# Kernel tuning notes

Measured on AMD Instinct MI355X. Metric: run time of the kernel, lower is better.

Reference implementation:

```python
import jax, jax.numpy as jnp
import numpy as np

NUM_HEADS = 16
DIM = 1024
N_TOKENS = 2048
S0 = 8            # number of frames
P = N_TOKENS // S0  # tokens per frame
B = 1


def setup_inputs() -> dict:
    key = jax.random.key(0)
    ks = jax.random.split(key, 8)
    C = DIM
    x = jax.random.normal(ks[0], (B, N_TOKENS, C), dtype=jnp.float32)
    # nn.Linear-style weights (out_features, in_features), scaled ~1/sqrt(fan_in)
    Wqkv = jax.random.normal(ks[1], (3 * C, C), dtype=jnp.float32) * (C ** -0.5)
    bqkv = jnp.zeros((3 * C,), dtype=jnp.float32)
    Wproj = jax.random.normal(ks[2], (C, C), dtype=jnp.float32) * (C ** -0.5)
    bproj = jnp.zeros((C,), dtype=jnp.float32)
    frame_bias = jax.random.normal(ks[3], (S0, S0), dtype=jnp.float32) * 0.5
    # frame adjacency: random sparsity pattern, diagonal always allowed
    adj = jax.random.bernoulli(ks[4], 0.25, (S0, S0))
    adj = adj | jnp.eye(S0, dtype=bool)
    frame_ids = (jnp.arange(N_TOKENS) // P).astype(jnp.int64)
    is_hub = jax.random.bernoulli(ks[5], 0.05, (N_TOKENS,))
    return {
        'x': x, 'Wqkv': Wqkv, 'bqkv': bqkv, 'Wproj': Wproj, 'bproj': bproj,
        'frame_bias': frame_bias, 'adj': adj, 'frame_ids': frame_ids,
        'is_hub': is_hub,
    }


def _sparse_attention(x, Wqkv, bqkv, Wproj, bproj, frame_bias, adj, frame_ids, is_hub):
    Bx, N, C = x.shape
    H = NUM_HEADS
    D = C // H
    scale = D ** -0.5
    # qkv projection -> q,k,v each [B,H,N,D]
    qkv = x @ Wqkv.T + bqkv                      # [B,N,3C]
    qkv = qkv.reshape(Bx, N, 3, H, D).transpose(2, 0, 3, 1, 4)
    q, k, v = qkv[0], qkv[1], qkv[2]

    # token-level mask derived from frame-level structures (score_mod semantics)
    fi = frame_ids                               # [N]
    adj_allowed = adj[fi[:, None], fi[None, :]]  # [N,N] bool
    same_frame = fi[:, None] == fi[None, :]
    neither_hub = ~(is_hub[:, None] | is_hub[None, :])
    hub_allowed = same_frame | neither_hub       # mask_hub_tokens=True
    allowed = adj_allowed & hub_allowed
    bias = frame_bias[fi[:, None], fi[None, :]]  # soft_mask=True

    scores = jnp.einsum('bhqd,bhkd->bhqk', q, k) * scale
    scores = jnp.where(allowed, scores + bias, -jnp.inf)
    attn = jax.nn.softmax(scores, axis=-1)
    out = jnp.einsum('bhqk,bhkd->bhqd', attn, v)
    out = out.transpose(0, 2, 1, 3).reshape(Bx, N, C)
    return out @ Wproj.T + bproj


def reference(x, Wqkv, bqkv, Wproj, bproj, frame_bias, adj, frame_ids, is_hub):
    return _sparse_attention(x, Wqkv, bqkv, Wproj, bproj, frame_bias,
                             adj, frame_ids, is_hub)
```

## Files before the change

### kernel.cpp

```cpp
#include <hip/hip_runtime.h>
#include <hip/hip_bf16.h>
#include <math.h>

#define NTOK 2048
#define CDIM 1024
#define NHEAD 16
#define HDIM 64

typedef __attribute__((ext_vector_type(8))) short bf16x8;
typedef __attribute__((ext_vector_type(4))) float f32x4;
typedef __attribute__((ext_vector_type(4))) unsigned int u32x4;

__device__ inline unsigned short bf16_rn(float f) {
    unsigned int u = __float_as_uint(f);
    u += 0x7FFFu + ((u >> 16) & 1u);
    return (unsigned short)(u >> 16);
}

template <int N> __device__ inline void waitcnt_vm() {
    if constexpr (N == 0) asm volatile("s_waitcnt vmcnt(0)" ::: "memory");
    else if constexpr (N == 2) asm volatile("s_waitcnt vmcnt(2)" ::: "memory");
    else if constexpr (N == 3) asm volatile("s_waitcnt vmcnt(3)" ::: "memory");
}

__device__ inline void gload16(const void* g, void* l) {
    __builtin_amdgcn_global_load_lds((const __attribute__((address_space(1))) void*)g,
                                     (__attribute__((address_space(3))) void*)l,
                                     16, 0, 0);
}

__global__ __launch_bounds__(256) void conv3(const float* __restrict__ s0, unsigned short* __restrict__ h0, int nb0,
                                             const float* __restrict__ s1, unsigned short* __restrict__ h1, int nb1,
                                             const float* __restrict__ s2, unsigned short* __restrict__ h2) {
    int b = blockIdx.x;
    const float* s;
    unsigned short* hh;
    if (b < nb0) { s = s0; hh = h0; }
    else if (b < nb0 + nb1) { s = s1; hh = h1; b -= nb0; }
    else { s = s2; hh = h2; b -= nb0 + nb1; }
    const int i = b * 256 + threadIdx.x;
    float4 v = ((const float4*)s)[i];
    ushort4 h;
    h.x = bf16_rn(v.x); h.y = bf16_rn(v.y); h.z = bf16_rn(v.z); h.w = bf16_rn(v.w);
    ((ushort4*)hh)[i] = h;
}

template <int BM, int BN, int M, int N, int K, int MODE>
__global__ __launch_bounds__(256) void gemm_mfma(const unsigned short* __restrict__ Ah,
                                                 const unsigned short* __restrict__ Bh,
                                                 const float* __restrict__ bias,
                                                 float* __restrict__ C,
                                                 unsigned short* __restrict__ qfb,
                                                 unsigned short* __restrict__ kfb,
                                                 unsigned short* __restrict__ vfb) {
    constexpr int FM = BM / 32;
    constexpr int FN = BN / 32;
    constexpr int ASZ = BM * 32;
    constexpr int BSZ = BN * 32;
    constexpr int BUF = ASZ + BSZ;
    __shared__ unsigned short lds[2 * BUF];

    const int tid = threadIdx.x;
    const int lane = tid & 63;
    const int w = tid >> 6;
    const int m0 = blockIdx.y * BM;
    const int n0 = blockIdx.x * BN;
    const int wave_m = (w >> 1) * (BM / 2);
    const int wave_n = (w & 1) * (BN / 2);
    const int lr = lane & 15;
    const int kg_ = lane >> 4;
    const int srow = tid >> 2;
    const int scol = (tid & 3) * 8;

    const size_t aRow = (size_t)(m0 + srow) * K + scol;
    const size_t bRow = (size_t)(n0 + (srow & (BN - 1))) * K + scol;

    f32x4 acc[FM][FN];
#pragma unroll
    for (int i = 0; i < FM; ++i)
#pragma unroll
        for (int j = 0; j < FN; ++j) acc[i][j] = {0.f, 0.f, 0.f, 0.f};

    auto stage = [&](int buf, int k0) {
        unsigned short* bb = lds + buf * BUF;
#pragma unroll
        for (int j = 0; j < BM / 64; ++j) {
            const size_t ga = aRow + (size_t)j * 64 * K + k0;
            gload16(Ah + ga, bb + (srow + j * 64) * 32 + scol);
        }
#pragma unroll
        for (int j = 0; j < (BN + 63) / 64; ++j) {
            const size_t gb = bRow + (size_t)j * 64 * K + k0;
            gload16(Bh + gb, bb + ASZ + ((srow & (BN - 1)) + j * 64) * 32 + scol);
        }
    };

    stage(0, 0);
    constexpr int NL = BM / 64 + (BN + 63) / 64;
    constexpr int NT = K / 32;
    for (int t = 0; t < NT; ++t) {
        const int cur = t & 1;
        if (t + 1 < NT) {
            stage(cur ^ 1, (t + 1) * 32);
            waitcnt_vm<NL>();
        } else {
            waitcnt_vm<0>();
        }
        __builtin_amdgcn_s_barrier();

        const unsigned short* bb = lds + cur * BUF;
        bf16x8 ah[FM], bh[FN];
#pragma unroll
        for (int f = 0; f < FM; ++f)
            ah[f] = *(const bf16x8*)&bb[(wave_m + f * 16 + lr) * 32 + kg_ * 8];
#pragma unroll
        for (int f = 0; f < FN; ++f)
            bh[f] = *(const bf16x8*)&bb[ASZ + (wave_n + f * 16 + lr) * 32 + kg_ * 8];
        __builtin_amdgcn_s_setprio(1);
#pragma unroll
        for (int fm = 0; fm < FM; ++fm)
#pragma unroll
            for (int fn = 0; fn < FN; ++fn)
                acc[fm][fn] = __builtin_amdgcn_mfma_f32_16x16x32_bf16(ah[fm], bh[fn], acc[fm][fn], 0, 0, 0);
        __builtin_amdgcn_s_setprio(0);
        asm volatile("" ::: "memory");
        __builtin_amdgcn_s_barrier();
    }

    if constexpr (MODE == 2) {
        float bv[FN];
#pragma unroll
        for (int fn = 0; fn < FN; ++fn) bv[fn] = bias[n0 + wave_n + fn * 16 + lr];
#pragma unroll
        for (int fm = 0; fm < FM; ++fm) {
            const int row0 = m0 + wave_m + fm * 16 + kg_ * 4;
#pragma unroll
            for (int fn = 0; fn < FN; ++fn) {
                const int col = n0 + wave_n + fn * 16 + lr;
#pragma unroll
                for (int r = 0; r < 4; ++r)
                    C[(size_t)(row0 + r) * N + col] = acc[fm][fn][r] + bv[fn];
            }
        }
    } else {
        const int reg = n0 >> 10;
#pragma unroll
        for (int fn = 0; fn < FN; ++fn) {
            const int col = n0 + wave_n + fn * 16 + lr;
            const int head = (col >> 6) & 15;
            const int d = col & 63;
            const float bv = bias[col];
#pragma unroll
            for (int fm = 0; fm < FM; ++fm) {
                const int row0 = m0 + wave_m + fm * 16 + kg_ * 4;
                if (reg == 2) {
                    const int tok = row0;
                    const int tile = tok >> 6;
                    const int t6 = tok & 63;
                    const int c = t6 >> 5;
                    const int t5 = t6 & 31;
                    const int hi = (t5 >> 4) & 1;
                    const int kgv = (t5 >> 2) & 3;
                    const int fd = d >> 4;
                    const int lrv = d & 15;
                    ushort4 pk;
                    pk.x = bf16_rn(acc[fm][fn][0] + bv);
                    pk.y = bf16_rn(acc[fm][fn][1] + bv);
                    pk.z = bf16_rn(acc[fm][fn][2] + bv);
                    pk.w = bf16_rn(acc[fm][fn][3] + bv);
                    const size_t idx = (((size_t)((head * 32 + tile) * 2 + c) * 4 + fd) * 64 +
                                        (kgv * 16 + lrv)) * 8 + hi * 4;
                    *(ushort4*)&vfb[idx] = pk;
                } else if (reg == 1) {
                    const int dc = d >> 5;
                    const int kgq = (d >> 3) & 3;
                    const int e = d & 7;
#pragma unroll
                    for (int r = 0; r < 4; ++r) {
                        const int tok = row0 + r;
                        const int tile = tok >> 6;
                        const int fk = (tok >> 4) & 3;
                        const int lrk = tok & 15;
                        const size_t idx = (((size_t)((head * 32 + tile) * 4 + fk) * 2 + dc) * 64 +
                                            (kgq * 16 + lrk)) * 8 + e;
                        kfb[idx] = bf16_rn(acc[fm][fn][r] + bv);
                    }
                } else {
                    const int dc = d >> 5;
                    const int kgq = (d >> 3) & 3;
                    const int e = d & 7;
#pragma unroll
                    for (int r = 0; r < 4; ++r) {
                        const int tok = row0 + r;
                        const int q16i = tok >> 4;
                        const int lrk = tok & 15;
                        const size_t idx = (((size_t)(head * 128 + q16i) * 2 + dc) * 64 +
                                            (kgq * 16 + lrk)) * 8 + e;
                        qfb[idx] = bf16_rn((acc[fm][fn][r] + bv) * 0.125f);
                    }
                }
            }
        }
    }
}

__global__ __launch_bounds__(128, 4) void attn_mfma(const unsigned short* __restrict__ qfb,
                                                    const unsigned short* __restrict__ kfb,
                                                    const unsigned short* __restrict__ vfb,
                                                    const float* __restrict__ frame_bias,
                                                    const int* __restrict__ adj,
                                                    const int* __restrict__ is_hub,
                                                    unsigned short* __restrict__ ath) {
    __shared__ float sM[64][18];
    __shared__ int sList[32];
    __shared__ float sFB[8];
    __shared__ unsigned long long sHub[32];
    __shared__ int sNT;

    const int bid = blockIdx.x;
    const int r8 = bid & 7, tt = bid >> 3;
    const int q16 = tt & 127, hb = tt >> 7;
    const int h = r8 * 2 + hb;
    const int q0 = q16 * 16;

    const int tid = threadIdx.x;
    const int lane = tid & 63;
    const int w = tid >> 6;
    const int lr = lane & 15;
    const int kg = lane >> 4;
    const int fi = q0 >> 8;

    const unsigned short* qb = qfb + ((size_t)(h * 128 + q16) * 2) * 512;
    bf16x8 qh[2];
    qh[0] = *(const bf16x8*)&qb[lane * 8];
    qh[1] = *(const bf16x8*)&qb[512 + lane * 8];
    const bool hq = is_hub[q0 + lr] != 0;

#pragma unroll
    for (int i = 0; i < 16; ++i) {
        const int t2 = w * 16 + i;
        unsigned long long mb = __ballot(is_hub[t2 * 64 + lane] != 0);
        if (lane == 0) sHub[t2] = mb;
    }
    if (tid < 8) sFB[tid] = frame_bias[fi * 8 + tid];
    if (w == 0) {
        const bool ok = (lane < 32) && (adj[fi * 8 + ((lane & 31) >> 2)] != 0);
        const unsigned long long am = __ballot(ok);
        if (lane == 0) {
            int c = 0;
#pragma unroll 1
            for (int t2 = 0; t2 < 32; ++t2)
                if ((am >> t2) & 1ull) sList[c++] = t2;
            sNT = c;
        }
    }
    __syncthreads();
    const int nt = sNT;

    const unsigned short* kb = kfb + (size_t)(h * 32) * 4096;
    const unsigned short* vb = vfb + (size_t)(h * 32) * 4096;

    float m_i = -INFINITY, l_i = 0.f;
    f32x4 oacc[4];
#pragma unroll
    for (int fd = 0; fd < 4; ++fd) oacc[fd] = {0.f, 0.f, 0.f, 0.f};

#pragma unroll 1
    for (int i = w; i < nt; i += 2) {
        const int tile = sList[i];
        const size_t tbase = (size_t)tile * 4096 + lane * 8;
        const int fj = tile >> 2;
        const bool same = (fj == fi);
        const float biasv = sFB[fj];
        const unsigned long long hubmask = sHub[tile];

        bf16x8 kfr[4][2];
#pragma unroll
        for (int fk = 0; fk < 4; ++fk)
#pragma unroll
            for (int dc = 0; dc < 2; ++dc)
                kfr[fk][dc] = *(const bf16x8*)&kb[tbase + (fk * 2 + dc) * 512];

        f32x4 sacc[4];
#pragma unroll
        for (int fk = 0; fk < 4; ++fk) sacc[fk] = {0.f, 0.f, 0.f, 0.f};
        __builtin_amdgcn_s_setprio(1);
#pragma unroll
        for (int fk = 0; fk < 4; ++fk)
#pragma unroll
            for (int dc = 0; dc < 2; ++dc)
                sacc[fk] = __builtin_amdgcn_mfma_f32_16x16x32_bf16(kfr[fk][dc], qh[dc], sacc[fk], 0, 0, 0);
        __builtin_amdgcn_s_setprio(0);

        bf16x8 vfr[2][4];
#pragma unroll
        for (int c = 0; c < 2; ++c)
#pragma unroll
            for (int fd = 0; fd < 4; ++fd)
                vfr[c][fd] = *(const bf16x8*)&vb[tbase + (c * 4 + fd) * 512];

        float sv[4][4];
        float rmax = -INFINITY;
#pragma unroll
        for (int fk = 0; fk < 4; ++fk)
#pragma unroll
            for (int r = 0; r < 4; ++r) {
                float val = sacc[fk][r] + biasv;
                if (!same) {
                    const int k = fk * 16 + kg * 4 + r;
                    if (hq || ((hubmask >> k) & 1ull)) val = -INFINITY;
                }
                sv[fk][r] = val;
                rmax = fmaxf(rmax, val);
            }
        rmax = fmaxf(rmax, __shfl_xor(rmax, 16));
        rmax = fmaxf(rmax, __shfl_xor(rmax, 32));

        const float mn = fmaxf(m_i, rmax);
        const float alpha = (mn == -INFINITY) ? 1.f : __expf(m_i - mn);
        m_i = mn;

        float p4[4][4];
        float psum = 0.f;
#pragma unroll
        for (int fk = 0; fk < 4; ++fk)
#pragma unroll
            for (int r = 0; r < 4; ++r) {
                const float pv = (sv[fk][r] == -INFINITY) ? 0.f : __expf(sv[fk][r] - mn);
                p4[fk][r] = pv;
                psum += pv;
            }
        psum += __shfl_xor(psum, 16);
        psum += __shfl_xor(psum, 32);
        l_i = l_i * alpha + psum;
#pragma unroll
        for (int fd = 0; fd < 4; ++fd) {
            oacc[fd][0] *= alpha; oacc[fd][1] *= alpha;
            oacc[fd][2] *= alpha; oacc[fd][3] *= alpha;
        }

        unsigned int pc[4][2];
#pragma unroll
        for (int fk = 0; fk < 4; ++fk)
#pragma unroll
            for (int rp = 0; rp < 2; ++rp)
                pc[fk][rp] = (unsigned int)bf16_rn(p4[fk][2 * rp]) |
                             ((unsigned int)bf16_rn(p4[fk][2 * rp + 1]) << 16);
        __builtin_amdgcn_s_setprio(1);
#pragma unroll
        for (int c = 0; c < 2; ++c) {
            u32x4 pw = {pc[2 * c][0], pc[2 * c][1], pc[2 * c + 1][0], pc[2 * c + 1][1]};
            bf16x8 pbv = __builtin_bit_cast(bf16x8, pw);
#pragma unroll
            for (int fd = 0; fd < 4; ++fd)
                oacc[fd] = __builtin_amdgcn_mfma_f32_16x16x32_bf16(vfr[c][fd], pbv, oacc[fd], 0, 0, 0);
        }
        __builtin_amdgcn_s_setprio(0);
    }

    if (w == 1) {
        float* mp = &sM[lane][0];
        mp[0] = m_i;
        mp[1] = l_i;
#pragma unroll
        for (int fd = 0; fd < 4; ++fd)
#pragma unroll
            for (int r = 0; r < 4; ++r) mp[2 + fd * 4 + r] = oacc[fd][r];
    }
    __syncthreads();
    if (w == 0) {
        const float mb = sM[lane][0];
        const float lb = sM[lane][1];
        const float m = fmaxf(m_i, mb);
        const float aa = (m_i == -INFINITY) ? 0.f : __expf(m_i - m);
        const float ab = (mb == -INFINITY) ? 0.f : __expf(mb - m);
        const float inv = 1.f / (l_i * aa + lb * ab);
#pragma unroll
        for (int fd = 0; fd < 4; ++fd) {
            ushort4 h4;
            unsigned short hs[4];
#pragma unroll
            for (int r = 0; r < 4; ++r) {
                const float o = (oacc[fd][r] * aa + sM[lane][2 + fd * 4 + r] * ab) * inv;
                hs[r] = bf16_rn(o);
            }
            h4.x = hs[0]; h4.y = hs[1]; h4.z = hs[2]; h4.w = hs[3];
            const size_t idx = (size_t)(q0 + lr) * CDIM + h * 64 + fd * 16 + kg * 4;
            *(ushort4*)&ath[idx] = h4;
        }
    }
}

extern "C" void kernel_launch(void* const* d_in, const int* in_sizes, int n_in,
                              void* d_out, int out_size, void* d_ws, size_t ws_size,
                              hipStream_t stream) {
    const float* x          = (const float*)d_in[0];
    const float* Wqkv       = (const float*)d_in[1];
    const float* bqkv       = (const float*)d_in[2];
    const float* Wproj      = (const float*)d_in[3];
    const float* bproj      = (const float*)d_in[4];
    const float* frame_bias = (const float*)d_in[5];
    const int*   adj        = (const int*)d_in[6];
    const int*   is_hub     = (const int*)d_in[8];
    float* out = (float*)d_out;

    char* ws = (char*)d_ws;
    size_t off = 0;
    auto alloc_us = [&](size_t n) { unsigned short* p = (unsigned short*)(ws + off); off += n * 2; return p; };
    unsigned short* qfb = alloc_us((size_t)NHEAD * NTOK * HDIM);
    unsigned short* kfb = alloc_us((size_t)NHEAD * NTOK * HDIM);
    unsigned short* vfb = alloc_us((size_t)NHEAD * HDIM * NTOK);
    unsigned short* xh  = alloc_us((size_t)NTOK * CDIM);
    unsigned short* wqh = alloc_us((size_t)3 * CDIM * CDIM);
    unsigned short* wph = alloc_us((size_t)CDIM * CDIM);
    unsigned short* ath = alloc_us((size_t)NTOK * CDIM);

    const int nb_x = (NTOK * CDIM / 4) / 256;
    const int nb_wq = (3 * CDIM * CDIM / 4) / 256;
    const int nb_wp = (CDIM * CDIM / 4) / 256;
    conv3<<<nb_x + nb_wq + nb_wp, 256, 0, stream>>>(x, xh, nb_x,
                                                    Wqkv, wqh, nb_wq,
                                                    Wproj, wph);

    gemm_mfma<64, 128, NTOK, 3 * CDIM, CDIM, 1>
        <<<dim3((3 * CDIM) / 128, NTOK / 64), 256, 0, stream>>>(
            xh, wqh, bqkv, nullptr, qfb, kfb, vfb);
    attn_mfma<<<2048, 128, 0, stream>>>(qfb, kfb, vfb,
                                        frame_bias, adj, is_hub, ath);
    gemm_mfma<64, 64, NTOK, CDIM, CDIM, 2>
        <<<dim3(CDIM / 64, NTOK / 64), 256, 0, stream>>>(
            ath, wph, bproj, out, nullptr, nullptr, nullptr);
}
```

Baseline: 73.02 us.

## Double GEMM K-tile to 64 and use lazy softmax rescaling in attention

The MFMA GEMM now stages a K-slice of 64 per pipeline step instead of 32, which halves the number of barrier/wait iterations and issues two MFMA k-substeps per stage. The staging layout is changed to 8 threads per row, and the waitcnt thresholds are updated to match the new load counts. In the flash-attention loop, the running max and the rescaling of the accumulator are only updated when some lane's new max exceeds the old one by more than a threshold of 8, so exp/multiply work is skipped on most tiles. The larger tile doubles LDS use per block, which may reduce occupancy. The lazy rescale relies on the bounded exponent staying within fp32 and bf16 range.

```diff
diff --git a/kernel.cpp b/kernel.cpp
--- a/kernel.cpp
+++ b/kernel.cpp
@@ -19,8 +19,8 @@
 
 template <int N> __device__ inline void waitcnt_vm() {
     if constexpr (N == 0) asm volatile("s_waitcnt vmcnt(0)" ::: "memory");
-    else if constexpr (N == 2) asm volatile("s_waitcnt vmcnt(2)" ::: "memory");
-    else if constexpr (N == 3) asm volatile("s_waitcnt vmcnt(3)" ::: "memory");
+    else if constexpr (N == 4) asm volatile("s_waitcnt vmcnt(4)" ::: "memory");
+    else if constexpr (N == 6) asm volatile("s_waitcnt vmcnt(6)" ::: "memory");
 }
 
 __device__ inline void gload16(const void* g, void* l) {
@@ -53,10 +53,11 @@
                                                  unsigned short* __restrict__ qfb,
                                                  unsigned short* __restrict__ kfb,
                                                  unsigned short* __restrict__ vfb) {
+    constexpr int BK = 64;
     constexpr int FM = BM / 32;
     constexpr int FN = BN / 32;
-    constexpr int ASZ = BM * 32;
-    constexpr int BSZ = BN * 32;
+    constexpr int ASZ = BM * BK;
+    constexpr int BSZ = BN * BK;
     constexpr int BUF = ASZ + BSZ;
     __shared__ unsigned short lds[2 * BUF];
 
@@ -69,11 +70,11 @@
     const int wave_n = (w & 1) * (BN / 2);
     const int lr = lane & 15;
     const int kg_ = lane >> 4;
-    const int srow = tid >> 2;
-    const int scol = (tid & 3) * 8;
+    const int srow = tid >> 3;
+    const int scol = (tid & 7) * 8;
 
     const size_t aRow = (size_t)(m0 + srow) * K + scol;
-    const size_t bRow = (size_t)(n0 + (srow & (BN - 1))) * K + scol;
+    const size_t bRow = (size_t)(n0 + srow) * K + scol;
 
     f32x4 acc[FM][FN];
 #pragma unroll
@@ -84,24 +85,20 @@
     auto stage = [&](int buf, int k0) {
         unsigned short* bb = lds + buf * BUF;
 #pragma unroll
-        for (int j = 0; j < BM / 64; ++j) {
-            const size_t ga = aRow + (size_t)j * 64 * K + k0;
-            gload16(Ah + ga, bb + (srow + j * 64) * 32 + scol);
-        }
-#pragma unroll
-        for (int j = 0; j < (BN + 63) / 64; ++j) {
-            const size_t gb = bRow + (size_t)j * 64 * K + k0;
-            gload16(Bh + gb, bb + ASZ + ((srow & (BN - 1)) + j * 64) * 32 + scol);
-        }
+        for (int j = 0; j < BM / 32; ++j)
+            gload16(Ah + aRow + (size_t)j * 32 * K + k0, bb + (srow + j * 32) * BK + scol);
+#pragma unroll
+        for (int j = 0; j < BN / 32; ++j)
+            gload16(Bh + bRow + (size_t)j * 32 * K + k0, bb + ASZ + (srow + j * 32) * BK + scol);
     };
 
     stage(0, 0);
-    constexpr int NL = BM / 64 + (BN + 63) / 64;
-    constexpr int NT = K / 32;
+    constexpr int NL = BM / 32 + BN / 32;
+    constexpr int NT = K / BK;
     for (int t = 0; t < NT; ++t) {
         const int cur = t & 1;
         if (t + 1 < NT) {
-            stage(cur ^ 1, (t + 1) * 32);
+            stage(cur ^ 1, (t + 1) * BK);
             waitcnt_vm<NL>();
         } else {
             waitcnt_vm<0>();
@@ -109,19 +106,25 @@
         __builtin_amdgcn_s_barrier();
 
         const unsigned short* bb = lds + cur * BUF;
-        bf16x8 ah[FM], bh[FN];
+        bf16x8 ah[FM][2], bh[FN][2];
 #pragma unroll
         for (int f = 0; f < FM; ++f)
-            ah[f] = *(const bf16x8*)&bb[(wave_m + f * 16 + lr) * 32 + kg_ * 8];
+#pragma unroll
+            for (int ks = 0; ks < 2; ++ks)
+                ah[f][ks] = *(const bf16x8*)&bb[(wave_m + f * 16 + lr) * BK + ks * 32 + kg_ * 8];
 #pragma unroll
         for (int f = 0; f < FN; ++f)
-            bh[f] = *(const bf16x8*)&bb[ASZ + (wave_n + f * 16 + lr) * 32 + kg_ * 8];
+#pragma unroll
+            for (int ks = 0; ks < 2; ++ks)
+                bh[f][ks] = *(const bf16x8*)&bb[ASZ + (wave_n + f * 16 + lr) * BK + ks * 32 + kg_ * 8];
         __builtin_amdgcn_s_setprio(1);
 #pragma unroll
-        for (int fm = 0; fm < FM; ++fm)
-#pragma unroll
-            for (int fn = 0; fn < FN; ++fn)
-                acc[fm][fn] = __builtin_amdgcn_mfma_f32_16x16x32_bf16(ah[fm], bh[fn], acc[fm][fn], 0, 0, 0);
+        for (int ks = 0; ks < 2; ++ks)
+#pragma unroll
+            for (int fm = 0; fm < FM; ++fm)
+#pragma unroll
+                for (int fn = 0; fn < FN; ++fn)
+                    acc[fm][fn] = __builtin_amdgcn_mfma_f32_16x16x32_bf16(ah[fm][ks], bh[fn][ks], acc[fm][fn], 0, 0, 0);
         __builtin_amdgcn_s_setprio(0);
         asm volatile("" ::: "memory");
         __builtin_amdgcn_s_barrier();
@@ -316,9 +319,17 @@
         rmax = fmaxf(rmax, __shfl_xor(rmax, 16));
         rmax = fmaxf(rmax, __shfl_xor(rmax, 32));
 
-        const float mn = fmaxf(m_i, rmax);
-        const float alpha = (mn == -INFINITY) ? 1.f : __expf(m_i - mn);
-        m_i = mn;
+        if (!__all(rmax <= m_i + 8.f)) {
+            const float mn = fmaxf(m_i, rmax);
+            const float alpha = (m_i == -INFINITY) ? 0.f : __expf(m_i - mn);
+            m_i = mn;
+            l_i *= alpha;
+#pragma unroll
+            for (int fd = 0; fd < 4; ++fd) {
+                oacc[fd][0] *= alpha; oacc[fd][1] *= alpha;
+                oacc[fd][2] *= alpha; oacc[fd][3] *= alpha;
+            }
+        }
 
         float p4[4][4];
         float psum = 0.f;
@@ -326,18 +337,13 @@
         for (int fk = 0; fk < 4; ++fk)
 #pragma unroll
             for (int r = 0; r < 4; ++r) {
-                const float pv = (sv[fk][r] == -INFINITY) ? 0.f : __expf(sv[fk][r] - mn);
+                const float pv = (sv[fk][r] == -INFINITY) ? 0.f : __expf(sv[fk][r] - m_i);
                 p4[fk][r] = pv;
                 psum += pv;
             }
         psum += __shfl_xor(psum, 16);
         psum += __shfl_xor(psum, 32);
-        l_i = l_i * alpha + psum;
-#pragma unroll
-        for (int fd = 0; fd < 4; ++fd) {
-            oacc[fd][0] *= alpha; oacc[fd][1] *= alpha;
-            oacc[fd][2] *= alpha; oacc[fd][3] *= alpha;
-        }
+        l_i += psum;
 
         unsigned int pc[4][2];
 #pragma unroll
```

New measurement: 70.12 us. -4.0%, faster.
